# Performance work log

Measured on AMD Instinct MI355X. Metric: run time of the kernel, lower is better.

The kernel has to match this reference:

```python
import jax, jax.numpy as jnp
import numpy as np
from jax import lax

SEQ, BATCH, IN, HID, LAYERS = 1024, 64, 384, 384, 5


def setup_inputs() -> dict:
    key = jax.random.key(0)
    kx, kw, kb = jax.random.split(key, 3)
    x = jax.random.normal(kx, (SEQ, BATCH, IN), dtype=jnp.float32)
    # Each QRNN layer (window=1): Linear(in, 3*hidden). in == hidden == 384 for all layers.
    scale = 1.0 / np.sqrt(IN)
    Ws = jax.random.uniform(kw, (LAYERS, IN, 3 * HID), dtype=jnp.float32, minval=-scale, maxval=scale)
    bs = jax.random.uniform(kb, (LAYERS, 3 * HID), dtype=jnp.float32, minval=-scale, maxval=scale)
    return {"x": x, "Ws": Ws, "bs": bs}


def _fo_pool(F, Z):
    # c_t = F_t * Z_t + (1 - F_t) * c_{t-1}, c_0 = 0  (ForgetMult, hidden=None)
    # linear recurrence c_t = a_t * c_{t-1} + b_t solved with associative scan over time.
    a = 1.0 - F
    b = F * Z
    def comb(l, r):
        a1, b1 = l
        a2, b2 = r
        return a2 * a1, a2 * b1 + b2
    _, C = lax.associative_scan(comb, (a, b), axis=0)
    return C


def _qrnn_layer(h, W, b):
    Y = jnp.einsum('sbi,ij->sbj', h, W) + b  # (S, B, 3H)
    Z, F, O = jnp.split(Y, 3, axis=-1)
    Z = jnp.tanh(Z)
    F = jax.nn.sigmoid(F)
    C = _fo_pool(F, Z)
    return jax.nn.sigmoid(O) * C


def reference(x, Ws, bs):
    h = x
    for i in range(LAYERS):
        h = _qrnn_layer(h, Ws[i], bs[i])
    return h
```

## Files before the change

### kernel.cpp

```cpp
#include <hip/hip_runtime.h>
#include <hip/hip_bf16.h>
#include <stdint.h>

#define SEQ    1024
#define BATCH  64
#define DIN    384
#define HID    384
#define NLAYER 5

constexpr int Ncols = 3 * HID;
constexpr int Kdim  = DIN;

typedef __attribute__((ext_vector_type(8))) __bf16 bf16x8;
typedef __attribute__((ext_vector_type(4))) float  f32x4;
typedef unsigned int u32;
typedef uint16_t u16;

constexpr int WF_U4_PER_LAYER = 9 * 4 * 6 * 8 * 64;

__device__ __forceinline__ u16 f32_to_bf16_rn(float x) {
  u32 u = __float_as_uint(x);
  u += 0x7FFFu + ((u >> 16) & 1u);
  return (u16)(u >> 16);
}
__device__ __forceinline__ float bf16_to_f32(u16 h) {
  return __uint_as_float(((u32)h) << 16);
}
__device__ __forceinline__ float bflo(u32 p) { return __uint_as_float(p << 16); }
__device__ __forceinline__ float bfhi(u32 p) { return __uint_as_float(p & 0xFFFF0000u); }
__device__ __forceinline__ u32 packbf(float a, float b) {
  return (u32)f32_to_bf16_rn(a) | ((u32)f32_to_bf16_rn(b) << 16);
}
__device__ __forceinline__ void split2(float x, u16& hi, u16& lo) {
  u16 h = f32_to_bf16_rn(x);
  lo = f32_to_bf16_rn(x - bf16_to_f32(h));
  hi = h;
}

__device__ __forceinline__ void gload_lds16(const void* g, void* l) {
  __builtin_amdgcn_global_load_lds(
      (const __attribute__((address_space(1))) void*)g,
      (__attribute__((address_space(3))) void*)l, 16, 0, 0);
}

__global__ void k_prep_w(const float* __restrict__ W, uint4* __restrict__ wf) {
  __shared__ float lds[64][130];
  const int nt = blockIdx.x;
  const int kt = blockIdx.y;
  const int layer = blockIdx.z;
  const float* Wl = W + (size_t)layer * Kdim * Ncols + (size_t)kt * 64 * Ncols;
  const int tid = threadIdx.x;
  for (int e = tid; e < 64 * 128; e += 256) {
    const int kl = e >> 7, jj = e & 127;
    int j;
    if (nt < 6) j = (jj < 64) ? (nt * 64 + jj) : (384 + nt * 64 + jj - 64);
    else        j = 768 + (nt - 6) * 128 + jj;
    lds[kl][jj] = Wl[(size_t)kl * Ncols + j];
  }
  __syncthreads();
  #pragma unroll
  for (int i = 0; i < 8; ++i) {
    const int cid = i * 256 + tid;
    const int ws = cid >> 9;
    const int rem = cid & 511;
    const int c = rem >> 6;
    const int lane = rem & 63;
    const int ks = c >> 2, pl = (c >> 1) & 1, n = c & 1;
    int jj;
    if (nt < 6) jj = ws * 16 + (lane & 15) + (n ? 64 : 0);
    else        jj = ws * 32 + n * 16 + (lane & 15);
    const int kl = ks * 32 + (lane >> 4) * 8;
    u16 h[8];
    #pragma unroll
    for (int t = 0; t < 8; ++t) {
      u16 hi, lo; split2(lds[kl + t][jj], hi, lo);
      h[t] = pl ? lo : hi;
    }
    uint4 o;
    o.x = (u32)h[0] | ((u32)h[1] << 16);
    o.y = (u32)h[2] | ((u32)h[3] << 16);
    o.z = (u32)h[4] | ((u32)h[5] << 16);
    o.w = (u32)h[6] | ((u32)h[7] << 16);
    wf[((((size_t)layer * 9 + nt) * 4 + ws) * 48 + kt * 8 + c) * 64 + lane] = o;
  }
}

__global__ void k_prep_xg(const float* __restrict__ x, u32* __restrict__ ap,
                          int n8, int bgRow) {
  int i = blockIdx.x * blockDim.x + threadIdx.x;
  const int stride = gridDim.x * blockDim.x;
  const float4* x4 = (const float4*)x;
  for (; i < n8; i += stride) {
    const int rl = i / 48;
    const int k8 = i - rl * 48;
    const int b_local = rl >> 10, s = rl & 1023;
    const size_t src = (size_t)(s * 64 + bgRow + b_local) * 96 + k8 * 2;
    const float4 v0 = x4[src], v1 = x4[src + 1];
    uint4 o;
    o.x = packbf(v0.x, v0.y); o.y = packbf(v0.z, v0.w);
    o.z = packbf(v1.x, v1.y); o.w = packbf(v1.z, v1.w);
    ((uint4*)ap)[i] = o;
  }
}

__global__ __launch_bounds__(256, 2) void k_gemm(
    const u16* __restrict__ A,
    const bf16x8* __restrict__ Wf,
    const float* __restrict__ bias,
    u32* __restrict__ zf, u32* __restrict__ ov,
    float* __restrict__ compA, float* __restrict__ compB,
    int Mtiles, int NCHg)
{
  __shared__ char smem[32768];

  const int tid  = threadIdx.x;
  const int L = blockIdx.y * 9 + blockIdx.x;
  const int q = (9 * Mtiles) >> 3;
  const int nl = (L & 7) * q + (L >> 3);
  const int mt = nl / 9;
  const int nt = nl - mt * 9;
  const int m0 = mt * 128;

  const int wave = tid >> 6, lane = tid & 63;
  const int qv = lane >> 4;
  const int ln = lane & 15;

  float b0i, b1i;
  if (nt < 6) {
    const int hcol = nt * 64 + wave * 16 + ln;
    b0i = bias[hcol];
    b1i = bias[384 + hcol];
  } else {
    const int hb = (nt - 6) * 128 + wave * 32 + ln;
    b0i = bias[768 + hb];
    b1i = bias[768 + hb + 16];
  }
  f32x4 acc[8][2];
  #pragma unroll
  for (int m = 0; m < 8; ++m) {
    acc[m][0] = f32x4{b0i, b0i, b0i, b0i};
    acc[m][1] = f32x4{b1i, b1i, b1i, b1i};
  }

  const int sr   = tid >> 3;
  const int sseg = tid & 7;
  u32 abase[2];
  #pragma unroll
  for (int ks = 0; ks < 2; ++ks)
    abase[ks] = (u32)(ln * 128 + (((ks * 4 + qv) ^ (ln & 7)) * 16));
  const bf16x8* wbase = Wf + ((size_t)(nt * 4 + wave) * 48) * 64 + lane;

  bf16x8 Wcur[8], Wnxt[8];

  auto stageA = [&](int kt, int p) {
    #pragma unroll
    for (int i = 0; i < 4; ++i) {
      const int r = i * 32 + sr;
      const int seg = sseg ^ (r & 7);
      const size_t ea = (size_t)(m0 + r) * Kdim + kt * 64 + seg * 8;
      gload_lds16(A + ea, smem + p * 16384 + r * 128 + sseg * 16);
    }
  };

  stageA(0, 0);
  #pragma unroll
  for (int c = 0; c < 8; ++c) Wcur[c] = wbase[c * 64];
  __syncthreads();

  #pragma unroll
  for (int kt = 0; kt < 6; ++kt) {
    const int p = kt & 1;
    if (kt < 5) {
      stageA(kt + 1, p ^ 1);
      #pragma unroll
      for (int c = 0; c < 8; ++c) Wnxt[c] = wbase[((kt + 1) * 8 + c) * 64];
    }
    #pragma unroll
    for (int ks = 0; ks < 2; ++ks) {
      bf16x8 fA[8];
      #pragma unroll
      for (int m = 0; m < 8; ++m)
        fA[m] = *(const bf16x8*)(smem + p * 16384 + m * 2048 + abase[ks]);
      #pragma unroll
      for (int m = 0; m < 8; ++m) {
        acc[m][0] = __builtin_amdgcn_mfma_f32_16x16x32_bf16(fA[m], Wcur[ks * 4 + 0], acc[m][0], 0, 0, 0);
        acc[m][1] = __builtin_amdgcn_mfma_f32_16x16x32_bf16(fA[m], Wcur[ks * 4 + 1], acc[m][1], 0, 0, 0);
        acc[m][0] = __builtin_amdgcn_mfma_f32_16x16x32_bf16(fA[m], Wcur[ks * 4 + 2], acc[m][0], 0, 0, 0);
        acc[m][1] = __builtin_amdgcn_mfma_f32_16x16x32_bf16(fA[m], Wcur[ks * 4 + 3], acc[m][1], 0, 0, 0);
      }
    }
    if (kt < 5) {
      __syncthreads();
      #pragma unroll
      for (int c = 0; c < 8; ++c) Wcur[c] = Wnxt[c];
    }
  }

  if (nt < 6) {
    const int hcol = nt * 64 + wave * 16 + ln;
    float Arun = 1.f, Brun = 0.f;
    #pragma unroll
    for (int m = 0; m < 8; ++m) {
      float Aseg = 1.f, Bseg = 0.f;
      #pragma unroll
      for (int r = 0; r < 4; ++r) {
        const float vz = acc[m][0][r];
        const float vf = acc[m][1][r];
        const float z = fmaf(2.f, __builtin_amdgcn_rcpf(1.f + __expf(-2.f * vz)), -1.f);
        const float f = __builtin_amdgcn_rcpf(1.f + __expf(-vf));
        const float av = 1.f - f;
        const float bb = f * z;
        const int row = m * 16 + qv * 4 + r;
        zf[(size_t)(m0 + row) * 384 + hcol] = packbf(av, bb);
        Bseg = fmaf(av, Bseg, bb);
        Aseg *= av;
      }
      {
        const float Ao = __shfl_xor(Aseg, 16), Bo = __shfl_xor(Bseg, 16);
        const bool late = qv & 1;
        const float Ae = late ? Ao : Aseg, Be = late ? Bo : Bseg;
        const float Al = late ? Aseg : Ao, Bl = late ? Bseg : Bo;
        Aseg = Al * Ae; Bseg = fmaf(Al, Be, Bl);
      }
      {
        const float Ao = __shfl_xor(Aseg, 32), Bo = __shfl_xor(Bseg, 32);
        const bool late = (qv >> 1) & 1;
        const float Ae = late ? Ao : Aseg, Be = late ? Bo : Bseg;
        const float Al = late ? Aseg : Ao, Bl = late ? Bseg : Bo;
        Aseg = Al * Ae; Bseg = fmaf(Al, Be, Bl);
      }
      Brun = fmaf(Aseg, Brun, Bseg);
      Arun *= Aseg;
    }
    if (qv == 0) {
      const int b_local = mt >> 3, chunk = mt & 7;
      const int chg = b_local * 384 + hcol;
      compA[chunk * NCHg + chg] = Arun;
      compB[chunk * NCHg + chg] = Brun;
    }
  } else {
    const int hb = (nt - 6) * 128 + wave * 32 + ln;
    const int pos = ((hb >> 5) << 4) + (hb & 15);
    #pragma unroll
    for (int m = 0; m < 8; ++m)
      #pragma unroll
      for (int r = 0; r < 4; ++r) {
        const float s0 = __builtin_amdgcn_rcpf(1.f + __expf(-acc[m][0][r]));
        const float s1 = __builtin_amdgcn_rcpf(1.f + __expf(-acc[m][1][r]));
        const int row = m * 16 + qv * 4 + r;
        ov[(size_t)(m0 + row) * 192 + pos] = packbf(s0, s1);
      }
  }
}

template<int WM>
__global__ void k_scan(const u32* __restrict__ zfp, const u32* __restrict__ op,
                       const float* __restrict__ compA, const float* __restrict__ compB,
                       u32* __restrict__ anext, float* __restrict__ out,
                       int NCHg, int bgRow)
{
  const int ch = blockIdx.x * blockDim.x + threadIdx.x;
  if (ch >= NCHg) return;
  const int chunk = blockIdx.y;
  const int b_local = ch / 384;
  const int h = ch - b_local * 384;
  float c = 0.f;
  for (int q = 0; q < chunk; ++q)
    c = fmaf(compA[q * NCHg + ch], c, compB[q * NCHg + ch]);

  const int r0 = b_local * 1024 + chunk * 128;
  const size_t zbase = (size_t)r0 * 384 + h;
  const size_t obase = (size_t)r0 * 192 + (((h >> 5) << 4) + (h & 15));
  const int osel = (h >> 4) & 1;

  u32 ab0[8], ab1[8], ow0[8], ow1[8];
  #pragma unroll
  for (int u = 0; u < 8; ++u) {
    ab0[u] = zfp[zbase + (size_t)u * 384];
    ow0[u] = op[obase + (size_t)u * 192];
  }
  for (int t0 = 0; t0 < 128; t0 += 16) {
    const size_t zb = zbase + (size_t)t0 * 384;
    const size_t ob = obase + (size_t)t0 * 192;
    #pragma unroll
    for (int u = 0; u < 8; ++u) {
      ab1[u] = zfp[zb + (size_t)(u + 8) * 384];
      ow1[u] = op[ob + (size_t)(u + 8) * 192];
    }
    #pragma unroll
    for (int u = 0; u < 8; ++u) {
      c = fmaf(bflo(ab0[u]), c, bfhi(ab0[u]));
      const float o = osel ? bfhi(ow0[u]) : bflo(ow0[u]);
      const float hv = o * c;
      const int t = t0 + u;
      if (WM == 0) {
        const u32 me = (u32)f32_to_bf16_rn(hv);
        const u32 nb = (u32)__shfl_xor((int)me, 1);
        if (!(h & 1)) anext[(size_t)(r0 + t) * 192 + (h >> 1)] = me | (nb << 16);
      } else {
        out[(size_t)((chunk * 128 + t) * 64 + bgRow + b_local) * 384 + h] = hv;
      }
    }
    if (t0 + 16 < 128) {
      #pragma unroll
      for (int u = 0; u < 8; ++u) {
        ab0[u] = zfp[zb + (size_t)(u + 16) * 384];
        ow0[u] = op[ob + (size_t)(u + 16) * 192];
      }
    }
    #pragma unroll
    for (int u = 0; u < 8; ++u) {
      c = fmaf(bflo(ab1[u]), c, bfhi(ab1[u]));
      const float o = osel ? bfhi(ow1[u]) : bflo(ow1[u]);
      const float hv = o * c;
      const int t = t0 + u + 8;
      if (WM == 0) {
        const u32 me = (u32)f32_to_bf16_rn(hv);
        const u32 nb = (u32)__shfl_xor((int)me, 1);
        if (!(h & 1)) anext[(size_t)(r0 + t) * 192 + (h >> 1)] = me | (nb << 16);
      } else {
        out[(size_t)((chunk * 128 + t) * 64 + bgRow + b_local) * 384 + h] = hv;
      }
    }
  }
}

extern "C" void kernel_launch(void* const* d_in, const int* in_sizes, int n_in,
                              void* d_out, int out_size, void* d_ws, size_t ws_size,
                              hipStream_t stream) {
  const float* x  = (const float*)d_in[0];
  const float* Ws = (const float*)d_in[1];
  const float* bs = (const float*)d_in[2];
  float* out = (float*)d_out;

  const size_t wfbytes = (size_t)NLAYER * WF_U4_PER_LAYER * 16;
  int G = 64;
  for (int g = 1; g <= 64; g *= 2) {
    const int Bg_ = BATCH / g;
    const size_t MG_ = (size_t)SEQ * Bg_;
    size_t need = wfbytes
                + MG_ * Kdim * 2
                + MG_ * 384 * 4
                + MG_ * 192 * 4
                + 2 * (size_t)8 * Bg_ * 384 * 4
                + 16 * 256;
    if (need <= ws_size) { G = g; break; }
  }
  const int Bg = BATCH / G;
  const int MG = SEQ * Bg;
  const int NCHg = Bg * HID;
  const int Mtiles = MG / 128;

  char* p = (char*)d_ws;
  auto carve = [&](size_t bytes) -> char* {
    char* r = p; p += (bytes + 255) & ~(size_t)255; return r;
  };
  uint4* Wf = (uint4*)carve(wfbytes);
  u32* Ap  = (u32*)carve((size_t)MG * Kdim * 2);
  u32* zf  = (u32*)carve((size_t)MG * 384 * 4);
  u32* ov  = (u32*)carve((size_t)MG * 192 * 4);
  float* cA = (float*)carve((size_t)8 * NCHg * 4);
  float* cB = (float*)carve((size_t)8 * NCHg * 4);

  k_prep_w<<<dim3(9, 6, NLAYER), 256, 0, stream>>>(Ws, Wf);

  const int scanBlocks = (NCHg + 255) / 256;
  for (int bg = 0; bg < G; ++bg) {
    const int bgRow = bg * Bg;
    const int n8 = MG * (Kdim / 8);
    const int pblocks = (n8 + 255) / 256 < 4096 ? (n8 + 255) / 256 : 4096;
    k_prep_xg<<<pblocks, 256, 0, stream>>>(x, Ap, n8, bgRow);

    for (int layer = 0; layer < NLAYER; ++layer) {
      const bf16x8* wl = (const bf16x8*)(Wf + (size_t)layer * WF_U4_PER_LAYER);
      const float* bias = bs + layer * Ncols;
      k_gemm<<<dim3(9, Mtiles), 256, 0, stream>>>(
          (const u16*)Ap, wl, bias, zf, ov, cA, cB, Mtiles, NCHg);
      if (layer < NLAYER - 1)
        k_scan<0><<<dim3(scanBlocks, 8), 256, 0, stream>>>(
            zf, ov, cA, cB, Ap, out, NCHg, bgRow);
      else
        k_scan<1><<<dim3(scanBlocks, 8), 256, 0, stream>>>(
            zf, ov, cA, cB, Ap, out, NCHg, bgRow);
    }
  }
}
```

Before: 868.9 us.

## Triple-buffer GEMM A tiles with manual vmcnt waits and raise occupancy

Rewrites the GEMM main loop as a fully unrolled three-stage LDS pipeline. A tiles are prefetched two steps ahead, and raw s_waitcnt vmcnt plus s_barrier replace __syncthreads. Weight fragments are double-buffered in registers, MFMA sections run at raised wave priority, and launch bounds ask for three blocks per CU. The aim is to hide global load latency better, at the cost of more LDS per block and register pressure that could cause spills. Correctness depends on the hand-counted vmcnt values.

```diff
diff --git a/kernel.cpp b/kernel.cpp
--- a/kernel.cpp
+++ b/kernel.cpp
@@ -9,7 +9,7 @@
 #define NLAYER 5
 
 constexpr int Ncols = 3 * HID;
-constexpr int Kdim  = DIN;
+constexpr int Kdim  = 384;
 
 typedef __attribute__((ext_vector_type(8))) __bf16 bf16x8;
 typedef __attribute__((ext_vector_type(4))) float  f32x4;
@@ -103,7 +103,7 @@
   }
 }
 
-__global__ __launch_bounds__(256, 2) void k_gemm(
+__global__ __launch_bounds__(256, 3) void k_gemm(
     const u16* __restrict__ A,
     const bf16x8* __restrict__ Wf,
     const float* __restrict__ bias,
@@ -111,7 +111,7 @@
     float* __restrict__ compA, float* __restrict__ compB,
     int Mtiles, int NCHg)
 {
-  __shared__ char smem[32768];
+  __shared__ char smem[49152];
 
   const int tid  = threadIdx.x;
   const int L = blockIdx.y * 9 + blockIdx.x;
@@ -150,51 +150,61 @@
     abase[ks] = (u32)(ln * 128 + (((ks * 4 + qv) ^ (ln & 7)) * 16));
   const bf16x8* wbase = Wf + ((size_t)(nt * 4 + wave) * 48) * 64 + lane;
 
-  bf16x8 Wcur[8], Wnxt[8];
-
-  auto stageA = [&](int kt, int p) {
-    #pragma unroll
-    for (int i = 0; i < 4; ++i) {
-      const int r = i * 32 + sr;
-      const int seg = sseg ^ (r & 7);
-      const size_t ea = (size_t)(m0 + r) * Kdim + kt * 64 + seg * 8;
-      gload_lds16(A + ea, smem + p * 16384 + r * 128 + sseg * 16);
-    }
-  };
-
-  stageA(0, 0);
-  #pragma unroll
-  for (int c = 0; c < 8; ++c) Wcur[c] = wbase[c * 64];
-  __syncthreads();
-
-  #pragma unroll
-  for (int kt = 0; kt < 6; ++kt) {
-    const int p = kt & 1;
-    if (kt < 5) {
-      stageA(kt + 1, p ^ 1);
-      #pragma unroll
-      for (int c = 0; c < 8; ++c) Wnxt[c] = wbase[((kt + 1) * 8 + c) * 64];
-    }
-    #pragma unroll
-    for (int ks = 0; ks < 2; ++ks) {
-      bf16x8 fA[8];
-      #pragma unroll
-      for (int m = 0; m < 8; ++m)
-        fA[m] = *(const bf16x8*)(smem + p * 16384 + m * 2048 + abase[ks]);
-      #pragma unroll
-      for (int m = 0; m < 8; ++m) {
-        acc[m][0] = __builtin_amdgcn_mfma_f32_16x16x32_bf16(fA[m], Wcur[ks * 4 + 0], acc[m][0], 0, 0, 0);
-        acc[m][1] = __builtin_amdgcn_mfma_f32_16x16x32_bf16(fA[m], Wcur[ks * 4 + 1], acc[m][1], 0, 0, 0);
-        acc[m][0] = __builtin_amdgcn_mfma_f32_16x16x32_bf16(fA[m], Wcur[ks * 4 + 2], acc[m][0], 0, 0, 0);
-        acc[m][1] = __builtin_amdgcn_mfma_f32_16x16x32_bf16(fA[m], Wcur[ks * 4 + 3], acc[m][1], 0, 0, 0);
-      }
-    }
-    if (kt < 5) {
-      __syncthreads();
-      #pragma unroll
-      for (int c = 0; c < 8; ++c) Wcur[c] = Wnxt[c];
-    }
-  }
+  bf16x8 W[2][8];
+
+#define STAGE(KT, P)                                                          \
+  {                                                                           \
+    _Pragma("unroll")                                                         \
+    for (int i = 0; i < 4; ++i) {                                             \
+      const int r = i * 32 + sr;                                              \
+      const int seg = sseg ^ (r & 7);                                         \
+      const size_t ea = (size_t)(m0 + r) * Kdim + (KT) * 64 + seg * 8;        \
+      gload_lds16(A + ea, smem + (P) * 16384 + r * 128 + sseg * 16);          \
+    }                                                                         \
+  }
+
+#define LOADW(KT, WP)                                                         \
+  {                                                                           \
+    _Pragma("unroll")                                                         \
+    for (int c = 0; c < 8; ++c) W[WP][c] = wbase[((KT) * 8 + c) * 64];        \
+  }
+
+#define COMPUTE(P, WP)                                                        \
+  {                                                                           \
+    __builtin_amdgcn_s_setprio(1);                                            \
+    _Pragma("unroll")                                                         \
+    for (int ks = 0; ks < 2; ++ks) {                                          \
+      bf16x8 fA[8];                                                           \
+      _Pragma("unroll")                                                       \
+      for (int m = 0; m < 8; ++m)                                             \
+        fA[m] = *(const bf16x8*)(smem + (P) * 16384 + m * 2048 + abase[ks]);  \
+      _Pragma("unroll")                                                       \
+      for (int m = 0; m < 8; ++m) {                                           \
+        acc[m][0] = __builtin_amdgcn_mfma_f32_16x16x32_bf16(fA[m], W[WP][ks * 4 + 0], acc[m][0], 0, 0, 0); \
+        acc[m][1] = __builtin_amdgcn_mfma_f32_16x16x32_bf16(fA[m], W[WP][ks * 4 + 1], acc[m][1], 0, 0, 0); \
+        acc[m][0] = __builtin_amdgcn_mfma_f32_16x16x32_bf16(fA[m], W[WP][ks * 4 + 2], acc[m][0], 0, 0, 0); \
+        acc[m][1] = __builtin_amdgcn_mfma_f32_16x16x32_bf16(fA[m], W[WP][ks * 4 + 3], acc[m][1], 0, 0, 0); \
+      }                                                                       \
+    }                                                                         \
+    __builtin_amdgcn_s_setprio(0);                                            \
+  }
+
+#define WAITBAR(N)                                                            \
+  asm volatile("s_waitcnt vmcnt(" #N ")" ::: "memory");                       \
+  asm volatile("s_barrier" ::: "memory");
+
+  STAGE(0, 0); STAGE(1, 1); LOADW(0, 0);
+  WAITBAR(12); STAGE(2, 2); LOADW(1, 1); COMPUTE(0, 0);
+  WAITBAR(20); STAGE(3, 0); LOADW(2, 0); COMPUTE(1, 1);
+  WAITBAR(20); STAGE(4, 1); LOADW(3, 1); COMPUTE(2, 0);
+  WAITBAR(20); STAGE(5, 2); LOADW(4, 0); COMPUTE(0, 1);
+  WAITBAR(20); LOADW(5, 1); COMPUTE(1, 0);
+  WAITBAR(16); COMPUTE(2, 1);
+
+#undef STAGE
+#undef LOADW
+#undef COMPUTE
+#undef WAITBAR
 
   if (nt < 6) {
     const int hcol = nt * 64 + wave * 16 + ln;
```

After: 844.6 us. -2.8%, faster.
